# Kernel optimization log

Hardware: AMD Instinct MI355X
Metric: run time of the kernel (lower is better)

The kernel has to match this reference:

```python
import jax, jax.numpy as jnp
import numpy as np

NEG_SLOPE = 0.2  # PyG GATConv default


def gat_layer(x, W, att_src, att_dst, bias, src, dst, concat):
    # x: [N, F_in]; W: [F_in, H*C]; att_src/att_dst: [H, C]; bias: [H*C] or [C]
    N = x.shape[0]
    H, C = att_src.shape
    h = (x @ W).reshape(N, H, C)                       # [N, H, C]
    a_s = jnp.einsum('nhc,hc->nh', h, att_src)         # [N, H]
    a_d = jnp.einsum('nhc,hc->nh', h, att_dst)
    e = jax.nn.leaky_relu(a_s[src] + a_d[dst], NEG_SLOPE)  # [E, H]
    # segment softmax over incoming edges of each destination node
    m = jax.ops.segment_max(e, dst, num_segments=N)
    m = jnp.where(jnp.isfinite(m), m, 0.0)
    ee = jnp.exp(e - m[dst])
    s = jax.ops.segment_sum(ee, dst, num_segments=N)
    alpha = ee / (s[dst] + 1e-16)                      # [E, H]
    out = jax.ops.segment_sum(h[src] * alpha[:, :, None], dst, num_segments=N)  # [N, H, C]
    out = out.reshape(N, H * C) if concat else out.mean(axis=1)
    return out + bias


def setup_inputs() -> dict:
    key = jax.random.key(0)
    ks = jax.random.split(key, 16)
    N, E, F_IN, NC = 100000, 3200000, 256, 40
    H, C = 8, 8  # hidden GATConv: heads=8, out=8 -> width 64
    inp = {}
    inp['features'] = jax.random.normal(ks[0], (N, F_IN), dtype=jnp.float32)
    inp['edge_index'] = jax.random.randint(ks[1], (2, E), 0, N, dtype=jnp.int64)
    def p(k, shape):
        return jax.random.normal(k, shape, dtype=jnp.float32) * 0.1
    # layer 0: in 256 -> 8 heads x 8 (concat -> 64)
    inp['W0'] = p(ks[2], (F_IN, H * C)); inp['as0'] = p(ks[3], (H, C)); inp['ad0'] = p(ks[4], (H, C)); inp['b0'] = jnp.zeros((H * C,), jnp.float32)
    # layer 1: 64 -> 8 heads x 8 (concat -> 64)
    inp['W1'] = p(ks[5], (H * C, H * C)); inp['as1'] = p(ks[6], (H, C)); inp['ad1'] = p(ks[7], (H, C)); inp['b1'] = jnp.zeros((H * C,), jnp.float32)
    # layer 2: 64 -> 1 head x n_classes (mean/no-concat)
    inp['W2'] = p(ks[8], (H * C, NC)); inp['as2'] = p(ks[9], (1, NC)); inp['ad2'] = p(ks[10], (1, NC)); inp['b2'] = jnp.zeros((NC,), jnp.float32)
    return inp


def reference(features, edge_index, W0, as0, ad0, b0, W1, as1, ad1, b1, W2, as2, ad2, b2):
    N = features.shape[0]
    loops = jnp.arange(N, dtype=edge_index.dtype)  # PyG GATConv adds self-loops by default
    src = jnp.concatenate([edge_index[0], loops])
    dst = jnp.concatenate([edge_index[1], loops])
    x = gat_layer(features, W0, as0, ad0, b0, src, dst, True)
    x = gat_layer(x, W1, as1, ad1, b1, src, dst, True)
    x = gat_layer(x, W2, as2, ad2, b2, src, dst, False)
    return jax.nn.log_softmax(x, axis=-1)
```

## Files before the change

kernel.cpp:

```cpp
#include <hip/hip_runtime.h>
#include <hip/hip_bf16.h>

#define NEG_SLOPE 0.2f
#define LOG2E 1.44269504f
#define EPB 4096

typedef __attribute__((ext_vector_type(8))) short short8;
typedef __attribute__((ext_vector_type(4))) float f32x4;

__device__ __forceinline__ unsigned short f2bf(float x) {
    unsigned u = __float_as_uint(x);
    unsigned r = (u + 0x7FFFu + ((u >> 16) & 1u)) >> 16;
    return (unsigned short)r;
}

__device__ __forceinline__ float fexp2(float x) {
    return __builtin_amdgcn_exp2f(x);
}

__device__ __forceinline__ float readlane_f(float v, int l) {
    return __int_as_float(__builtin_amdgcn_readlane(__float_as_int(v), l));
}


__global__ __launch_bounds__(256) void bucket_hist_k(
    const int* __restrict__ dsts, int* __restrict__ bcnt, int E, int Etot,
    int nbuck) {
    __shared__ int lh[512];
    for (int i = threadIdx.x; i < nbuck; i += 256) lh[i] = 0;
    __syncthreads();
    int base = blockIdx.x * EPB;
    int cnt = Etot - base;
    if (cnt > EPB) cnt = EPB;
    for (int i = threadIdx.x; i < cnt; i += 256) {
        int e = base + i;
        int d = (e < E) ? dsts[e] : (e - E);
        atomicAdd(&lh[d >> 8], 1);
    }
    __syncthreads();
    for (int i = threadIdx.x; i < nbuck; i += 256) {
        int c = lh[i];
        if (c) atomicAdd(&bcnt[i], c);
    }
}

__global__ __launch_bounds__(512) void bucket_scan_k(
    const int* __restrict__ bcnt, int* __restrict__ bptr,
    int* __restrict__ bcur, int nbuck, int Etot) {
    __shared__ int tmp[512];
    int t = threadIdx.x;
    int v = (t < nbuck) ? bcnt[t] : 0;
    tmp[t] = v;
    __syncthreads();
    for (int off = 1; off < 512; off <<= 1) {
        int x = (t >= off) ? tmp[t - off] : 0;
        __syncthreads();
        tmp[t] += x;
        __syncthreads();
    }
    int excl = tmp[t] - v;
    if (t < nbuck) { bptr[t] = excl; bcur[t] = excl; }
    if (t == 0) bptr[nbuck] = Etot;
}

__global__ __launch_bounds__(256) void bucket_scatter_k(
    const int* __restrict__ srcs, const int* __restrict__ dsts,
    int* __restrict__ bcur, int2* __restrict__ pairs, int E, int Etot,
    int nbuck) {
    __shared__ int lh[512];
    __shared__ int lbase[512];
    for (int i = threadIdx.x; i < nbuck; i += 256) lh[i] = 0;
    __syncthreads();
    int base = blockIdx.x * EPB;
    int cnt = Etot - base;
    if (cnt > EPB) cnt = EPB;
    for (int i = threadIdx.x; i < cnt; i += 256) {
        int e = base + i;
        int d = (e < E) ? dsts[e] : (e - E);
        atomicAdd(&lh[d >> 8], 1);
    }
    __syncthreads();
    for (int i = threadIdx.x; i < nbuck; i += 256) {
        int c = lh[i];
        lbase[i] = c ? atomicAdd(&bcur[i], c) : 0;
    }
    __syncthreads();
    for (int i = threadIdx.x; i < nbuck; i += 256) lh[i] = 0;
    __syncthreads();
    for (int i = threadIdx.x; i < cnt; i += 256) {
        int e = base + i;
        int s, d;
        if (e < E) { s = srcs[e]; d = dsts[e]; }
        else       { s = e - E;   d = s; }
        int b = d >> 8;
        int off = atomicAdd(&lh[b], 1);
        pairs[lbase[b] + off] = make_int2(s, d);
    }
}

__global__ __launch_bounds__(256) void bucket_sort_k(
    const int2* __restrict__ pairs, const int* __restrict__ bptr,
    int* __restrict__ row_ptr, int* __restrict__ csr_src, int N, int Etot,
    int nbuck) {
    __shared__ int lh[256];
    __shared__ int lscan[256];
    int b = blockIdx.x;
    int n0 = b << 8;
    int e0 = bptr[b], e1 = bptr[b + 1];
    int t = threadIdx.x;
    lh[t] = 0;
    __syncthreads();
    for (int e = e0 + t; e < e1; e += 256)
        atomicAdd(&lh[pairs[e].y - n0], 1);
    __syncthreads();
    int v = lh[t];
    lscan[t] = v;
    __syncthreads();
    for (int off = 1; off < 256; off <<= 1) {
        int x = (t >= off) ? lscan[t - off] : 0;
        __syncthreads();
        lscan[t] += x;
        __syncthreads();
    }
    int start = e0 + lscan[t] - v;
    int n = n0 + t;
    if (n < N) row_ptr[n] = start;
    lh[t] = start;
    __syncthreads();
    for (int e = e0 + t; e < e1; e += 256) {
        int2 p = pairs[e];
        int pos = atomicAdd(&lh[p.y - n0], 1);
        csr_src[pos] = p.x;
    }
    if (b == nbuck - 1 && t == 0) row_ptr[N] = Etot;
}


template <int K>
__global__ __launch_bounds__(256) void gemm_pack8_k(
    const float* __restrict__ x, const float* __restrict__ W,
    const float* __restrict__ a_src, const float* __restrict__ a_dst,
    char* __restrict__ rec, float* __restrict__ adb, int N) {
    constexpr int NT = 4;
    constexpr int KT = K / 32;
    constexpr size_t WF_BYTES = (size_t)KT * NT * 64 * 8 * sizeof(short);
    constexpr size_t H_BYTES = (size_t)64 * 65 * sizeof(float);
    __shared__ alignas(16) char smem[WF_BYTES > H_BYTES ? WF_BYTES : H_BYTES];
    short* Wf = (short*)smem;
    float* hL = (float*)smem;
    int tid = threadIdx.x;
    for (int f = tid; f < KT * NT * 64; f += 256) {
        int lane = f & 63;
        int ntk = f >> 6;
        int nt = ntk % NT, kt = ntk / NT;
        int q = lane >> 4, c = lane & 15;
        int n = nt * 16 + c;
        int k0 = kt * 32 + q * 8;
        short8 frag;
        #pragma unroll
        for (int j = 0; j < 8; ++j)
            frag[j] = (short)f2bf(W[(size_t)(k0 + j) * 64 + n]);
        *(short8*)&Wf[f * 8] = frag;
    }
    __syncthreads();
    int wave = tid >> 6, lane = tid & 63;
    int q = lane >> 4, c = lane & 15;
    int m0 = blockIdx.x * 64 + wave * 16;
    int arow = m0 + c;
    int arl = arow < N ? arow : N - 1;
    f32x4 acc[NT] = {};
    for (int kt = 0; kt < KT; ++kt) {
        const float* xp = x + (size_t)arl * K + kt * 32 + q * 8;
        float4 a0 = *(const float4*)xp;
        float4 a1 = *(const float4*)(xp + 4);
        float av[8] = {a0.x, a0.y, a0.z, a0.w, a1.x, a1.y, a1.z, a1.w};
        short8 af;
        #pragma unroll
        for (int j = 0; j < 8; ++j) af[j] = (short)f2bf(av[j]);
        #pragma unroll
        for (int nt = 0; nt < NT; ++nt) {
            short8 bf = *(const short8*)&Wf[((kt * NT + nt) * 64 + lane) * 8];
            acc[nt] = __builtin_amdgcn_mfma_f32_16x16x32_bf16(af, bf, acc[nt],
                                                              0, 0, 0);
        }
    }
    __syncthreads();
    int lrow = wave * 16 + q * 4;
    #pragma unroll
    for (int nt = 0; nt < NT; ++nt)
        #pragma unroll
        for (int reg = 0; reg < 4; ++reg)
            hL[(lrow + reg) * 65 + nt * 16 + c] = acc[nt][reg];
    __syncthreads();
    #pragma unroll
    for (int it = 0; it < 2; ++it) {
        int id = it * 256 + tid;
        int ln = id >> 3, hd = id & 7;
        int gn = blockIdx.x * 64 + ln;
        if (gn >= N) continue;
        const float* hp = &hL[ln * 65 + hd * 8];
        float as = 0.f, ad = 0.f;
        float hv[8];
        #pragma unroll
        for (int j = 0; j < 8; ++j) {
            hv[j] = hp[j];
            as += hv[j] * a_src[hd * 8 + j];
            ad += hv[j] * a_dst[hd * 8 + j];
        }
        adb[gn * 8 + hd] = ad * LOG2E;
        char* r = rec + (size_t)gn * 192;
        unsigned short u[8];
        #pragma unroll
        for (int j = 0; j < 8; ++j) u[j] = f2bf(hv[j]);
        uint4 pk;
        pk.x = (unsigned)u[0] | ((unsigned)u[1] << 16);
        pk.y = (unsigned)u[2] | ((unsigned)u[3] << 16);
        pk.z = (unsigned)u[4] | ((unsigned)u[5] << 16);
        pk.w = (unsigned)u[6] | ((unsigned)u[7] << 16);
        *(uint4*)(r + hd * 16) = pk;
        *(float*)(r + 128 + hd * 4) = as * LOG2E;
    }
}


__global__ __launch_bounds__(256) void gemm_pack40_k(
    const float* __restrict__ x, const float* __restrict__ W,
    const float* __restrict__ a_src, const float* __restrict__ a_dst,
    char* __restrict__ rec, float* __restrict__ adb, int N) {
    constexpr int K = 64, NT = 3, KT = 2;
    constexpr size_t WF_BYTES = (size_t)KT * NT * 64 * 8 * sizeof(short);
    constexpr size_t H_BYTES = (size_t)64 * 41 * sizeof(float);
    __shared__ alignas(16) char smem[WF_BYTES > H_BYTES ? WF_BYTES : H_BYTES];
    short* Wf = (short*)smem;
    float* hL = (float*)smem;
    int tid = threadIdx.x;
    for (int f = tid; f < KT * NT * 64; f += 256) {
        int lane = f & 63;
        int ntk = f >> 6;
        int nt = ntk % NT, kt = ntk / NT;
        int q = lane >> 4, c = lane & 15;
        int n = nt * 16 + c;
        int k0 = kt * 32 + q * 8;
        short8 frag;
        #pragma unroll
        for (int j = 0; j < 8; ++j) {
            float v = (n < 40) ? W[(size_t)(k0 + j) * 40 + n] : 0.f;
            frag[j] = (short)f2bf(v);
        }
        *(short8*)&Wf[f * 8] = frag;
    }
    __syncthreads();
    int wave = tid >> 6, lane = tid & 63;
    int q = lane >> 4, c = lane & 15;
    int m0 = blockIdx.x * 64 + wave * 16;
    int arow = m0 + c;
    int arl = arow < N ? arow : N - 1;
    f32x4 acc[NT] = {};
    for (int kt = 0; kt < KT; ++kt) {
        const float* xp = x + (size_t)arl * K + kt * 32 + q * 8;
        float4 a0 = *(const float4*)xp;
        float4 a1 = *(const float4*)(xp + 4);
        float av[8] = {a0.x, a0.y, a0.z, a0.w, a1.x, a1.y, a1.z, a1.w};
        short8 af;
        #pragma unroll
        for (int j = 0; j < 8; ++j) af[j] = (short)f2bf(av[j]);
        #pragma unroll
        for (int nt = 0; nt < NT; ++nt) {
            short8 bf = *(const short8*)&Wf[((kt * NT + nt) * 64 + lane) * 8];
            acc[nt] = __builtin_amdgcn_mfma_f32_16x16x32_bf16(af, bf, acc[nt],
                                                              0, 0, 0);
        }
    }
    __syncthreads();
    int lrow = wave * 16 + q * 4;
    #pragma unroll
    for (int nt = 0; nt < NT; ++nt) {
        int n = nt * 16 + c;
        if (n >= 40) continue;
        #pragma unroll
        for (int reg = 0; reg < 4; ++reg)
            hL[(lrow + reg) * 41 + n] = acc[nt][reg];
    }
    __syncthreads();
    int ln = tid >> 2, sub = tid & 3;
    int gn = blockIdx.x * 64 + ln;
    float pas = 0.f, pad = 0.f;
    if (gn < N) {
        for (int j = sub; j < 40; j += 4) {
            float hv = hL[ln * 41 + j];
            pas += hv * a_src[j];
            pad += hv * a_dst[j];
        }
    }
    pas += __shfl_xor(pas, 1); pas += __shfl_xor(pas, 2);
    pad += __shfl_xor(pad, 1); pad += __shfl_xor(pad, 2);
    if (gn < N && sub == 0) {
        *(float*)(rec + (size_t)gn * 128 + 80) = pas * LOG2E;
        adb[gn] = pad * LOG2E;
    }
    for (int i = tid; i < 64 * 40; i += 256) {
        int n2 = i / 40, ch = i % 40;
        int g2 = blockIdx.x * 64 + n2;
        if (g2 < N)
            *(unsigned short*)(rec + (size_t)g2 * 128 + ch * 2) =
                f2bf(hL[n2 * 41 + ch]);
    }
}


#define EDGE64(SUF, IDX)                                                     \
    int s##SUF = __builtin_amdgcn_readlane(sv, (IDX));                       \
    const char* r##SUF = rec + (size_t)s##SUF * 192;                         \
    float a##SUF = *(const float*)(r##SUF + hoff);                           \
    unsigned u##SUF = *(const unsigned short*)(r##SUF + lane2);              \
    float v##SUF = a##SUF + ad;                                              \
    v##SUF = fmaxf(v##SUF, NEG_SLOPE * v##SUF);                              \
    float w##SUF = fexp2(v##SUF);

__global__ __launch_bounds__(256) void aggr64_k(
    const char* __restrict__ rec, const float* __restrict__ adb,
    const int* __restrict__ row_ptr, const int* __restrict__ csr_src,
    const float* __restrict__ bias, float* __restrict__ out, int N) {
    int node = blockIdx.x * 4 + (threadIdx.x >> 6);
    if (node >= N) return;
    int lane = threadIdx.x & 63;
    int hd = lane >> 3;
    int lane2 = lane * 2;
    int hoff = 128 + hd * 4;
    int beg = row_ptr[node], end = row_ptr[node + 1];
    float ad = adb[node * 8 + hd];
    float acc0 = 0.f, acc1 = 0.f, acc2 = 0.f, acc3 = 0.f;
    float acc4 = 0.f, acc5 = 0.f, acc6 = 0.f, acc7 = 0.f;
    float l0 = 0.f, l1 = 0.f, l2 = 0.f, l3 = 0.f;
    float l4 = 0.f, l5 = 0.f, l6 = 0.f, l7 = 0.f;
    for (int i0 = beg; i0 < end; i0 += 64) {
        int tail = end - i0;
        int sv = csr_src[i0 + (lane < tail ? lane : 0)];
        int cnt = tail < 64 ? tail : 64;
        int j = 0;
        for (; j + 8 <= cnt; j += 8) {
            EDGE64(A, j)     EDGE64(B, j + 1) EDGE64(C, j + 2) EDGE64(D, j + 3)
            EDGE64(E2, j + 4) EDGE64(F, j + 5) EDGE64(G, j + 6) EDGE64(H2, j + 7)
            l0 += wA; l1 += wB; l2 += wC; l3 += wD;
            l4 += wE2; l5 += wF; l6 += wG; l7 += wH2;
            acc0 = fmaf(wA, __uint_as_float(uA << 16), acc0);
            acc1 = fmaf(wB, __uint_as_float(uB << 16), acc1);
            acc2 = fmaf(wC, __uint_as_float(uC << 16), acc2);
            acc3 = fmaf(wD, __uint_as_float(uD << 16), acc3);
            acc4 = fmaf(wE2, __uint_as_float(uE2 << 16), acc4);
            acc5 = fmaf(wF, __uint_as_float(uF << 16), acc5);
            acc6 = fmaf(wG, __uint_as_float(uG << 16), acc6);
            acc7 = fmaf(wH2, __uint_as_float(uH2 << 16), acc7);
        }
        for (; j + 4 <= cnt; j += 4) {
            EDGE64(A, j) EDGE64(B, j + 1) EDGE64(C, j + 2) EDGE64(D, j + 3)
            l0 += wA; l1 += wB; l2 += wC; l3 += wD;
            acc0 = fmaf(wA, __uint_as_float(uA << 16), acc0);
            acc1 = fmaf(wB, __uint_as_float(uB << 16), acc1);
            acc2 = fmaf(wC, __uint_as_float(uC << 16), acc2);
            acc3 = fmaf(wD, __uint_as_float(uD << 16), acc3);
        }
        for (; j < cnt; ++j) {
            EDGE64(A, j)
            l0 += wA;
            acc0 = fmaf(wA, __uint_as_float(uA << 16), acc0);
        }
    }
    float l = ((l0 + l1) + (l2 + l3)) + ((l4 + l5) + (l6 + l7));
    float acc = ((acc0 + acc1) + (acc2 + acc3)) + ((acc4 + acc5) + (acc6 + acc7));
    out[(size_t)node * 64 + lane] = acc / (l + 1e-16f) + bias[lane];
}


#define F40(SUF, IDX)                                                        \
    int s##SUF = __builtin_amdgcn_readlane(sv, (IDX));                       \
    float w##SUF = readlane_f(wv, (IDX));                                    \
    unsigned u##SUF =                                                        \
        *(const unsigned short*)(rec + (size_t)s##SUF * 128 + cl2);

__global__ __launch_bounds__(256) void aggr40_k(
    const char* __restrict__ rec, const float* __restrict__ adb,
    const int* __restrict__ row_ptr, const int* __restrict__ csr_src,
    const float* __restrict__ bias, float* __restrict__ out, int N) {
    int node = blockIdx.x * 4 + (threadIdx.x >> 6);
    if (node >= N) return;
    int lane = threadIdx.x & 63;
    int cl2 = (lane < 40 ? lane : 0) * 2;
    int beg = row_ptr[node], end = row_ptr[node + 1];
    float ad = adb[node];
    float acc0 = 0.f, acc1 = 0.f, acc2 = 0.f, acc3 = 0.f;
    float acc4 = 0.f, acc5 = 0.f, acc6 = 0.f, acc7 = 0.f;
    float lpart = 0.f;
    for (int i0 = beg; i0 < end; i0 += 64) {
        int tail = end - i0;
        int sv = csr_src[i0 + (lane < tail ? lane : 0)];
        int cnt = tail < 64 ? tail : 64;
        float as = *(const float*)(rec + (size_t)sv * 128 + 80);
        float v = as + ad;
        v = fmaxf(v, NEG_SLOPE * v);
        float wv = fexp2(v);
        wv = (lane < cnt) ? wv : 0.f;
        lpart += wv;
        int j = 0;
        for (; j + 8 <= cnt; j += 8) {
            F40(A, j)     F40(B, j + 1) F40(C, j + 2) F40(D, j + 3)
            F40(E2, j + 4) F40(F, j + 5) F40(G, j + 6) F40(H2, j + 7)
            acc0 = fmaf(wA, __uint_as_float(uA << 16), acc0);
            acc1 = fmaf(wB, __uint_as_float(uB << 16), acc1);
            acc2 = fmaf(wC, __uint_as_float(uC << 16), acc2);
            acc3 = fmaf(wD, __uint_as_float(uD << 16), acc3);
            acc4 = fmaf(wE2, __uint_as_float(uE2 << 16), acc4);
            acc5 = fmaf(wF, __uint_as_float(uF << 16), acc5);
            acc6 = fmaf(wG, __uint_as_float(uG << 16), acc6);
            acc7 = fmaf(wH2, __uint_as_float(uH2 << 16), acc7);
        }
        for (; j + 4 <= cnt; j += 4) {
            F40(A, j) F40(B, j + 1) F40(C, j + 2) F40(D, j + 3)
            acc0 = fmaf(wA, __uint_as_float(uA << 16), acc0);
            acc1 = fmaf(wB, __uint_as_float(uB << 16), acc1);
            acc2 = fmaf(wC, __uint_as_float(uC << 16), acc2);
            acc3 = fmaf(wD, __uint_as_float(uD << 16), acc3);
        }
        for (; j < cnt; ++j) {
            F40(A, j)
            acc0 = fmaf(wA, __uint_as_float(uA << 16), acc0);
        }
    }
    #pragma unroll
    for (int off = 32; off > 0; off >>= 1) lpart += __shfl_xor(lpart, off);
    float l = lpart;
    float acc = ((acc0 + acc1) + (acc2 + acc3)) + ((acc4 + acc5) + (acc6 + acc7));
    float val = acc / (l + 1e-16f) + ((lane < 40) ? bias[lane] : 0.f);
    float mval = (lane < 40) ? val : -1e30f;
    #pragma unroll
    for (int off = 32; off > 0; off >>= 1)
        mval = fmaxf(mval, __shfl_xor(mval, off));
    float ex = (lane < 40) ? __expf(val - mval) : 0.f;
    #pragma unroll
    for (int off = 32; off > 0; off >>= 1) ex += __shfl_xor(ex, off);
    if (lane < 40)
        out[(size_t)node * 40 + lane] = val - mval - __logf(ex);
}


extern "C" void kernel_launch(void* const* d_in, const int* in_sizes, int n_in,
                              void* d_out, int out_size, void* d_ws,
                              size_t ws_size, hipStream_t stream) {
    const float* features = (const float*)d_in[0];
    const int* edge_index = (const int*)d_in[1];
    const float* W0 = (const float*)d_in[2];
    const float* as0 = (const float*)d_in[3];
    const float* ad0 = (const float*)d_in[4];
    const float* b0 = (const float*)d_in[5];
    const float* W1 = (const float*)d_in[6];
    const float* as1 = (const float*)d_in[7];
    const float* ad1 = (const float*)d_in[8];
    const float* b1 = (const float*)d_in[9];
    const float* W2 = (const float*)d_in[10];
    const float* as2 = (const float*)d_in[11];
    const float* ad2 = (const float*)d_in[12];
    const float* b2 = (const float*)d_in[13];

    int N = in_sizes[0] / 256;
    int E = in_sizes[1] / 2;
    int Etot = E + N;
    int nbuck = (N + 255) >> 8;
    const int* srcs = edge_index;
    const int* dsts = edge_index + E;

    float* ws = (float*)d_ws;
    float* Hbuf = ws;
    float* Abuf = Hbuf + (size_t)N * 64;
    float* adb  = Abuf + (size_t)N * 64;
    char* recbuf = (char*)(adb + (size_t)N * 8);
    int* row_ptr = (int*)(recbuf + (size_t)N * 192);
    int* bcnt    = row_ptr + (N + 2);
    int* bptr    = bcnt + 512;
    int* bcur    = bptr + 513;
    int* csr_src = bcur + 512;
    int2* pairs  = (int2*)Hbuf;

    const int B = 256;
    int gAg = (N + 3) / 4;
    int gBk = (Etot + EPB - 1) / EPB;
    int gGm = (N + 63) / 64;

    (void)hipMemsetAsync(bcnt, 0, 512 * 4, stream);
    bucket_hist_k<<<gBk, B, 0, stream>>>(dsts, bcnt, E, Etot, nbuck);
    bucket_scan_k<<<1, 512, 0, stream>>>(bcnt, bptr, bcur, nbuck, Etot);
    bucket_scatter_k<<<gBk, B, 0, stream>>>(srcs, dsts, bcur, pairs, E, Etot,
                                            nbuck);
    bucket_sort_k<<<nbuck, B, 0, stream>>>(pairs, bptr, row_ptr, csr_src, N,
                                           Etot, nbuck);

    gemm_pack8_k<256><<<gGm, B, 0, stream>>>(features, W0, as0, ad0, recbuf,
                                             adb, N);
    aggr64_k<<<gAg, B, 0, stream>>>(recbuf, adb, row_ptr, csr_src, b0, Abuf,
                                    N);

    gemm_pack8_k<64><<<gGm, B, 0, stream>>>(Abuf, W1, as1, ad1, recbuf, adb,
                                            N);
    aggr64_k<<<gAg, B, 0, stream>>>(recbuf, adb, row_ptr, csr_src, b1, Abuf,
                                    N);

    gemm_pack40_k<<<gGm, B, 0, stream>>>(Abuf, W2, as2, ad2, recbuf, adb, N);
    aggr40_k<<<gAg, B, 0, stream>>>(recbuf, adb, row_ptr, csr_src, b2,
                                    (float*)d_out, N);
}
```

Baseline: 652.3 us.

## Split attention scores from feature records and precompute edge weights into LDS

The packed per-node record (bf16 features plus attention scores, 192 bytes) is split into a 128-byte feature array and a separate per-node source-score array, and the 40-class record shrinks to 80 bytes. In the 64-wide aggregation, each lane now loads all 8 head scores for one edge, computes the 8 exp weights in parallel and writes them to a double-buffered LDS table. The inner loop then reads weights from LDS instead of doing a per-edge gather and exp on every lane. This cuts redundant exp work and reduces the gather footprint, at the cost of LDS traffic and no explicit barrier between write and read within a wave.

```diff
diff --git a/kernel.cpp b/kernel.cpp
--- a/kernel.cpp
+++ b/kernel.cpp
@@ -140,7 +140,8 @@
 __global__ __launch_bounds__(256) void gemm_pack8_k(
     const float* __restrict__ x, const float* __restrict__ W,
     const float* __restrict__ a_src, const float* __restrict__ a_dst,
-    char* __restrict__ rec, float* __restrict__ adb, int N) {
+    char* __restrict__ hrec, float* __restrict__ asb,
+    float* __restrict__ adb, int N) {
     constexpr int NT = 4;
     constexpr int KT = K / 32;
     constexpr size_t WF_BYTES = (size_t)KT * NT * 64 * 8 * sizeof(short);
@@ -208,7 +209,7 @@
             ad += hv[j] * a_dst[hd * 8 + j];
         }
         adb[gn * 8 + hd] = ad * LOG2E;
-        char* r = rec + (size_t)gn * 192;
+        asb[gn * 8 + hd] = as * LOG2E;
         unsigned short u[8];
         #pragma unroll
         for (int j = 0; j < 8; ++j) u[j] = f2bf(hv[j]);
@@ -217,8 +218,7 @@
         pk.y = (unsigned)u[2] | ((unsigned)u[3] << 16);
         pk.z = (unsigned)u[4] | ((unsigned)u[5] << 16);
         pk.w = (unsigned)u[6] | ((unsigned)u[7] << 16);
-        *(uint4*)(r + hd * 16) = pk;
-        *(float*)(r + 128 + hd * 4) = as * LOG2E;
+        *(uint4*)(hrec + (size_t)gn * 128 + hd * 16) = pk;
     }
 }
 
@@ -226,7 +226,8 @@
 __global__ __launch_bounds__(256) void gemm_pack40_k(
     const float* __restrict__ x, const float* __restrict__ W,
     const float* __restrict__ a_src, const float* __restrict__ a_dst,
-    char* __restrict__ rec, float* __restrict__ adb, int N) {
+    char* __restrict__ h40, float* __restrict__ asb40,
+    float* __restrict__ adb, int N) {
     constexpr int K = 64, NT = 3, KT = 2;
     constexpr size_t WF_BYTES = (size_t)KT * NT * 64 * 8 * sizeof(short);
     constexpr size_t H_BYTES = (size_t)64 * 41 * sizeof(float);
@@ -295,14 +296,14 @@
     pas += __shfl_xor(pas, 1); pas += __shfl_xor(pas, 2);
     pad += __shfl_xor(pad, 1); pad += __shfl_xor(pad, 2);
     if (gn < N && sub == 0) {
-        *(float*)(rec + (size_t)gn * 128 + 80) = pas * LOG2E;
+        asb40[gn] = pas * LOG2E;
         adb[gn] = pad * LOG2E;
     }
     for (int i = tid; i < 64 * 40; i += 256) {
         int n2 = i / 40, ch = i % 40;
         int g2 = blockIdx.x * 64 + n2;
         if (g2 < N)
-            *(unsigned short*)(rec + (size_t)g2 * 128 + ch * 2) =
+            *(unsigned short*)(h40 + (size_t)g2 * 80 + ch * 2) =
                 f2bf(hL[n2 * 41 + ch]);
     }
 }
@@ -310,36 +311,64 @@
 
 #define EDGE64(SUF, IDX)                                                     \
     int s##SUF = __builtin_amdgcn_readlane(sv, (IDX));                       \
-    const char* r##SUF = rec + (size_t)s##SUF * 192;                         \
-    float a##SUF = *(const float*)(r##SUF + hoff);                           \
-    unsigned u##SUF = *(const unsigned short*)(r##SUF + lane2);              \
-    float v##SUF = a##SUF + ad;                                              \
-    v##SUF = fmaxf(v##SUF, NEG_SLOPE * v##SUF);                              \
-    float w##SUF = fexp2(v##SUF);
+    float w##SUF = lwp[(IDX)];                                               \
+    unsigned u##SUF =                                                        \
+        *(const unsigned short*)(hrec + (size_t)s##SUF * 128 + lane2);
 
 __global__ __launch_bounds__(256) void aggr64_k(
-    const char* __restrict__ rec, const float* __restrict__ adb,
-    const int* __restrict__ row_ptr, const int* __restrict__ csr_src,
-    const float* __restrict__ bias, float* __restrict__ out, int N) {
-    int node = blockIdx.x * 4 + (threadIdx.x >> 6);
+    const char* __restrict__ hrec, const float* __restrict__ asb,
+    const float* __restrict__ adb, const int* __restrict__ row_ptr,
+    const int* __restrict__ csr_src, const float* __restrict__ bias,
+    float* __restrict__ out, int N) {
+    __shared__ float wlds[4 * 1040];
+    int wave = threadIdx.x >> 6;
+    int node = blockIdx.x * 4 + wave;
     if (node >= N) return;
     int lane = threadIdx.x & 63;
     int hd = lane >> 3;
     int lane2 = lane * 2;
-    int hoff = 128 + hd * 4;
+    float* wbA = wlds + wave * 1040;
+    float* wbB = wbA + 520;
+    const float* lwpA = wbA + hd * 65;
+    const float* lwpB = wbB + hd * 65;
     int beg = row_ptr[node], end = row_ptr[node + 1];
-    float ad = adb[node * 8 + hd];
+    float4 adv0 = *(const float4*)(adb + (size_t)node * 8);
+    float4 adv1 = *(const float4*)(adb + (size_t)node * 8 + 4);
     float acc0 = 0.f, acc1 = 0.f, acc2 = 0.f, acc3 = 0.f;
     float acc4 = 0.f, acc5 = 0.f, acc6 = 0.f, acc7 = 0.f;
     float l0 = 0.f, l1 = 0.f, l2 = 0.f, l3 = 0.f;
     float l4 = 0.f, l5 = 0.f, l6 = 0.f, l7 = 0.f;
-    for (int i0 = beg; i0 < end; i0 += 64) {
+    int par = 0;
+    for (int i0 = beg; i0 < end; i0 += 64, par ^= 1) {
         int tail = end - i0;
         int sv = csr_src[i0 + (lane < tail ? lane : 0)];
         int cnt = tail < 64 ? tail : 64;
+        float* wb = par ? wbB : wbA;
+        const float* lwp = par ? lwpB : lwpA;
+        {
+            const float* asp = asb + (size_t)sv * 8;
+            float4 s0 = *(const float4*)asp;
+            float4 s1 = *(const float4*)(asp + 4);
+            float w0 = s0.x + adv0.x; w0 = fmaxf(w0, NEG_SLOPE * w0); w0 = fexp2(w0);
+            float w1 = s0.y + adv0.y; w1 = fmaxf(w1, NEG_SLOPE * w1); w1 = fexp2(w1);
+            float w2 = s0.z + adv0.z; w2 = fmaxf(w2, NEG_SLOPE * w2); w2 = fexp2(w2);
+            float w3 = s0.w + adv0.w; w3 = fmaxf(w3, NEG_SLOPE * w3); w3 = fexp2(w3);
+            float w4 = s1.x + adv1.x; w4 = fmaxf(w4, NEG_SLOPE * w4); w4 = fexp2(w4);
+            float w5 = s1.y + adv1.y; w5 = fmaxf(w5, NEG_SLOPE * w5); w5 = fexp2(w5);
+            float w6 = s1.z + adv1.z; w6 = fmaxf(w6, NEG_SLOPE * w6); w6 = fexp2(w6);
+            float w7 = s1.w + adv1.w; w7 = fmaxf(w7, NEG_SLOPE * w7); w7 = fexp2(w7);
+            wb[lane]       = w0;
+            wb[65 + lane]  = w1;
+            wb[130 + lane] = w2;
+            wb[195 + lane] = w3;
+            wb[260 + lane] = w4;
+            wb[325 + lane] = w5;
+            wb[390 + lane] = w6;
+            wb[455 + lane] = w7;
+        }
         int j = 0;
         for (; j + 8 <= cnt; j += 8) {
-            EDGE64(A, j)     EDGE64(B, j + 1) EDGE64(C, j + 2) EDGE64(D, j + 3)
+            EDGE64(A, j)      EDGE64(B, j + 1) EDGE64(C, j + 2) EDGE64(D, j + 3)
             EDGE64(E2, j + 4) EDGE64(F, j + 5) EDGE64(G, j + 6) EDGE64(H2, j + 7)
             l0 += wA; l1 += wB; l2 += wC; l3 += wD;
             l4 += wE2; l5 += wF; l6 += wG; l7 += wH2;
@@ -376,12 +405,13 @@
     int s##SUF = __builtin_amdgcn_readlane(sv, (IDX));                       \
     float w##SUF = readlane_f(wv, (IDX));                                    \
     unsigned u##SUF =                                                        \
-        *(const unsigned short*)(rec + (size_t)s##SUF * 128 + cl2);
+        *(const unsigned short*)(hrec + (size_t)s##SUF * 80 + cl2);
 
 __global__ __launch_bounds__(256) void aggr40_k(
-    const char* __restrict__ rec, const float* __restrict__ adb,
-    const int* __restrict__ row_ptr, const int* __restrict__ csr_src,
-    const float* __restrict__ bias, float* __restrict__ out, int N) {
+    const char* __restrict__ hrec, const float* __restrict__ asb,
+    const float* __restrict__ adb, const int* __restrict__ row_ptr,
+    const int* __restrict__ csr_src, const float* __restrict__ bias,
+    float* __restrict__ out, int N) {
     int node = blockIdx.x * 4 + (threadIdx.x >> 6);
     if (node >= N) return;
     int lane = threadIdx.x & 63;
@@ -395,7 +425,7 @@
         int tail = end - i0;
         int sv = csr_src[i0 + (lane < tail ? lane : 0)];
         int cnt = tail < 64 ? tail : 64;
-        float as = *(const float*)(rec + (size_t)sv * 128 + 80);
+        float as = asb[sv];
         float v = as + ad;
         v = fmaxf(v, NEG_SLOPE * v);
         float wv = fexp2(v);
@@ -472,8 +502,9 @@
     float* Hbuf = ws;
     float* Abuf = Hbuf + (size_t)N * 64;
     float* adb  = Abuf + (size_t)N * 64;
-    char* recbuf = (char*)(adb + (size_t)N * 8);
-    int* row_ptr = (int*)(recbuf + (size_t)N * 192);
+    float* asb  = adb + (size_t)N * 8;
+    char* hrec  = (char*)(asb + (size_t)N * 8);
+    int* row_ptr = (int*)(hrec + (size_t)N * 128);
     int* bcnt    = row_ptr + (N + 2);
     int* bptr    = bcnt + 512;
     int* bcur    = bptr + 513;
@@ -493,17 +524,18 @@
     bucket_sort_k<<<nbuck, B, 0, stream>>>(pairs, bptr, row_ptr, csr_src, N,
                                            Etot, nbuck);
 
-    gemm_pack8_k<256><<<gGm, B, 0, stream>>>(features, W0, as0, ad0, recbuf,
-                                             adb, N);
-    aggr64_k<<<gAg, B, 0, stream>>>(recbuf, adb, row_ptr, csr_src, b0, Abuf,
-                                    N);
-
-    gemm_pack8_k<64><<<gGm, B, 0, stream>>>(Abuf, W1, as1, ad1, recbuf, adb,
-                                            N);
-    aggr64_k<<<gAg, B, 0, stream>>>(recbuf, adb, row_ptr, csr_src, b1, Abuf,
-                                    N);
-
-    gemm_pack40_k<<<gGm, B, 0, stream>>>(Abuf, W2, as2, ad2, recbuf, adb, N);
-    aggr40_k<<<gAg, B, 0, stream>>>(recbuf, adb, row_ptr, csr_src, b2,
+    gemm_pack8_k<256><<<gGm, B, 0, stream>>>(features, W0, as0, ad0, hrec,
+                                             asb, adb, N);
+    aggr64_k<<<gAg, B, 0, stream>>>(hrec, asb, adb, row_ptr, csr_src, b0,
+                                    Abuf, N);
+
+    gemm_pack8_k<64><<<gGm, B, 0, stream>>>(Abuf, W1, as1, ad1, hrec, asb,
+                                            adb, N);
+    aggr64_k<<<gAg, B, 0, stream>>>(hrec, asb, adb, row_ptr, csr_src, b1,
+                                    Abuf, N);
+
+    gemm_pack40_k<<<gGm, B, 0, stream>>>(Abuf, W2, as2, ad2, hrec, asb, adb,
+                                         N);
+    aggr40_k<<<gAg, B, 0, stream>>>(hrec, asb, adb, row_ptr, csr_src, b2,
                                     (float*)d_out, N);
 }
```

Measured after the change: 622.8 us. 1.05x faster.
